# Optimization experiments

Hardware: AMD Instinct MI355X
Metric: run time of the kernel (lower is better)

Reference implementation:

```python
import jax, jax.numpy as jnp
import numpy as np

DIM = 1024
HEADS = 16
SCALE = DIM ** -0.5  # note: source scales by full dim, not head dim


def setup_inputs() -> dict:
    key = jax.random.key(0)
    k1, k2, k3 = jax.random.split(key, 3)
    b, n = 2, 2048
    x = jax.random.normal(k1, (b, n, DIM), dtype=jnp.float32)
    w_qkv = jax.random.normal(k2, (3 * DIM, DIM), dtype=jnp.float32) * (DIM ** -0.5)
    w_out = jax.random.normal(k3, (DIM, DIM), dtype=jnp.float32) * (DIM ** -0.5)
    b_out = jnp.zeros((DIM,), dtype=jnp.float32)
    return {"x": x, "w_qkv": w_qkv, "w_out": w_out, "b_out": b_out}


def reference(x, w_qkv, w_out, b_out):
    b, n, d = x.shape
    h = HEADS
    hd = d // h
    # torch Linear: y = x @ W.T
    qkv = x @ w_qkv.T  # [b, n, 3d]
    q, k, v = jnp.split(qkv, 3, axis=-1)
    # reshape to [b, h, n, hd]
    def to_heads(t):
        return t.reshape(b, n, h, hd).transpose(0, 2, 1, 3)
    q, k, v = to_heads(q), to_heads(k), to_heads(v)
    dots = jnp.einsum('bhqd,bhkd->bhqk', q, k) * SCALE
    attn = jax.nn.softmax(dots, axis=-1)
    out = jnp.einsum('bhqk,bhkd->bhqd', attn, v)
    out = out.transpose(0, 2, 1, 3).reshape(b, n, d)
    return out @ w_out.T + b_out
```

## Files before the change

### kernel.cpp

```cpp
#include <hip/hip_runtime.h>

typedef __attribute__((ext_vector_type(8))) _Float16 half8;
typedef __attribute__((ext_vector_type(4))) _Float16 half4;
typedef __attribute__((ext_vector_type(2))) __fp16 fp16x2;
typedef __attribute__((ext_vector_type(4))) float f32x4;
typedef __attribute__((ext_vector_type(4))) unsigned int u32x4;
typedef __attribute__((ext_vector_type(2))) unsigned int u32x2;

#define NSEQ 2048
#define DIMM 1024
#define NH   16
#define HD   64

typedef const void __attribute__((address_space(1))) gvoid_t;
typedef void __attribute__((address_space(3))) svoid_t;

__device__ __forceinline__ void gload_lds16(const void* g, void* l) {
  __builtin_amdgcn_global_load_lds((gvoid_t*)g, (svoid_t*)l, 16, 0, 0);
}

union H2U { fp16x2 h; unsigned int u; };

__global__ __launch_bounds__(256) void cvt_all(const float* __restrict__ x,
                                               const float* __restrict__ wqkv,
                                               const float* __restrict__ wout,
                                               _Float16* __restrict__ xh,
                                               _Float16* __restrict__ wqkvh,
                                               _Float16* __restrict__ wouth) {
  int i = blockIdx.x * 256 + threadIdx.x;
  const float* src;
  _Float16* dst;
  int off;
  if (i < 524288) { src = x; dst = xh; off = i; }
  else if (i < 917504) { src = wqkv; dst = wqkvh; off = i - 524288; }
  else { src = wout; dst = wouth; off = i - 917504; }
  const float4* p = (const float4*)src + (size_t)off * 2;
  float4 v0 = p[0], v1 = p[1];
  half8 h;
  h[0] = (_Float16)v0.x; h[1] = (_Float16)v0.y; h[2] = (_Float16)v0.z; h[3] = (_Float16)v0.w;
  h[4] = (_Float16)v1.x; h[5] = (_Float16)v1.y; h[6] = (_Float16)v1.z; h[7] = (_Float16)v1.w;
  *((half8*)dst + off) = h;
}

__device__ __forceinline__ void gemm_mainloop_q(const _Float16* __restrict__ A,
                                                const _Float16* __restrict__ B,
                                                int am0, int bn0,
                                                _Float16* As, _Float16* Bs,
                                                f32x4 acc[4][4]) {
  const int tid = threadIdx.x;
  const int w = tid >> 6, lane = tid & 63;
  const int lr = lane >> 2;
  const int lc = (lane & 3) * 8;
  const int wm = (w >> 1) * 64, wn = (w & 1) * 64;
  const int g = lane >> 4, ln = lane & 15;

#define GSTAGE_Q(buf, kk)                                                           \
  {                                                                                 \
    _Pragma("unroll")                                                               \
    for (int i = 0; i < 4; ++i) {                                                   \
      int c = w * 4 + i;                                                            \
      if (c < 8) {                                                                  \
        gload_lds16(A + (size_t)(am0 + c * 16 + lr) * 1024 + (kk) + lc,             \
                    As + (buf) * 4096 + c * 512);                                   \
      } else {                                                                      \
        int cb = c - 8;                                                             \
        gload_lds16(B + (size_t)(bn0 + cb * 16 + lr) * 1024 + (kk) + lc,            \
                    Bs + (buf) * 4096 + cb * 512);                                  \
      }                                                                             \
    }                                                                               \
  }

  GSTAGE_Q(0, 0)
  GSTAGE_Q(1, 32)
  for (int t = 0; t < 32; ++t) {
    if (t < 31) {
      asm volatile("s_waitcnt vmcnt(4)" ::: "memory");
    } else {
      asm volatile("s_waitcnt vmcnt(0)" ::: "memory");
    }
    __builtin_amdgcn_s_barrier();
    if (t < 30) GSTAGE_Q((t + 2) % 3, (t + 2) * 32);
    const _Float16* as_ = As + (t % 3) * 4096;
    const _Float16* bs_ = Bs + (t % 3) * 4096;
    half8 af[4], bf[4];
#pragma unroll
    for (int mi = 0; mi < 4; ++mi)
      af[mi] = *(const half8*)(as_ + (wm + mi * 16 + ln) * 32 + g * 8);
#pragma unroll
    for (int ni = 0; ni < 4; ++ni)
      bf[ni] = *(const half8*)(bs_ + (wn + ni * 16 + ln) * 32 + g * 8);
#pragma unroll
    for (int mi = 0; mi < 4; ++mi)
#pragma unroll
      for (int ni = 0; ni < 4; ++ni)
        acc[mi][ni] = __builtin_amdgcn_mfma_f32_16x16x32_f16(af[mi], bf[ni], acc[mi][ni], 0, 0, 0);
  }
}

union SmemQKV {
  struct { _Float16 a[3 * 128 * 32]; _Float16 b[3 * 128 * 32]; } ab;
  _Float16 t[128 * 136];
};

#define QSCALE 0.0450843450f

__global__ __launch_bounds__(256) void gemm_qkv(const _Float16* __restrict__ x,
                                                const _Float16* __restrict__ wqkv,
                                                _Float16* __restrict__ qh,
                                                _Float16* __restrict__ kh,
                                                _Float16* __restrict__ vt) {
  __shared__ SmemQKV sh;
  f32x4 acc[4][4];
#pragma unroll
  for (int i = 0; i < 4; ++i)
#pragma unroll
    for (int j = 0; j < 4; ++j) acc[i][j] = (f32x4){0.f, 0.f, 0.f, 0.f};
  const int bm = blockIdx.x, bn = blockIdx.y;
  gemm_mainloop_q(x, wqkv, bm * 128, bn * 128, sh.ab.a, sh.ab.b, acc);

  const int tid = threadIdx.x;
  const int w = tid >> 6, lane = tid & 63;
  const int g = lane >> 4, ln = lane & 15;
  const int wm = (w >> 1) * 64, wn = (w & 1) * 64;
  const int sec = bn >> 3;
  const int cbase = (bn & 7) * 128;

  if (sec < 2) {
    _Float16* dst = (sec == 0) ? qh : kh;
    const float scale = (sec == 0) ? QSCALE : 1.0f;
#pragma unroll
    for (int mi = 0; mi < 4; ++mi) {
      int row = bm * 128 + wm + mi * 16 + g * 4;
      int bidx = row >> 11, nidx = row & 2047;
#pragma unroll
      for (int ni = 0; ni < 4; ++ni) {
        int col = cbase + wn + ni * 16 + ln;
        int h = col >> 6, d = col & 63;
        _Float16* p = dst + ((size_t)(bidx * NH + h) * NSEQ + nidx) * HD + d;
#pragma unroll
        for (int r = 0; r < 4; ++r) p[r * HD] = (_Float16)(acc[mi][ni][r] * scale);
      }
    }
  } else {
    __syncthreads();
#pragma unroll
    for (int mi = 0; mi < 4; ++mi)
#pragma unroll
      for (int ni = 0; ni < 4; ++ni)
#pragma unroll
        for (int r = 0; r < 4; ++r)
          sh.t[(wn + ni * 16 + ln) * 136 + wm + mi * 16 + g * 4 + r] = (_Float16)acc[mi][ni][r];
    __syncthreads();
    const int row0 = bm * 128;
    const int bidx = row0 >> 11, n0 = row0 & 2047;
#pragma unroll
    for (int i = 0; i < 8; ++i) {
      int ci = i * 256 + tid;
      int drow = ci >> 4, nofs = (ci & 15) * 8;
      int col = cbase + drow;
      int h = col >> 6, d = col & 63;
      u32x4 val = *(const u32x4*)(sh.t + drow * 136 + nofs);
      *(u32x4*)(vt + ((size_t)(bidx * NH + h) * HD + d) * NSEQ + n0 + nofs) = val;
    }
  }
}

__global__ __launch_bounds__(256, 2) void attn_fwd(const _Float16* __restrict__ qg,
                                                   const _Float16* __restrict__ kg,
                                                   const _Float16* __restrict__ vg,
                                                   _Float16* __restrict__ ao) {
  __shared__ _Float16 Ks[3][64 * 64];
  __shared__ _Float16 Vs[3][64 * 64];
  __shared__ float Lred[2][128];

  const int bid = blockIdx.x;
  const int swz = (bid & 7) * 64 + (bid >> 3);
  const int bh = swz >> 4, qt = swz & 15;
  const int tid = threadIdx.x, w = tid >> 6, lane = tid & 63;
  const int g = lane >> 4, ln = lane & 15;
  const int sw8 = ln & 7;
  const int qh2 = w >> 1, kh2 = w & 1;

  const _Float16* qp = qg + (size_t)bh * NSEQ * HD;
  const _Float16* kp = kg + (size_t)bh * NSEQ * HD;
  const _Float16* vp = vg + (size_t)bh * HD * NSEQ;

  const int qr0 = qt * 128;

  half8 qf[4][2];
#pragma unroll
  for (int qb = 0; qb < 4; ++qb)
#pragma unroll
    for (int dk = 0; dk < 2; ++dk)
      qf[qb][dk] = *(const half8*)(qp + (size_t)(qr0 + qh2 * 64 + qb * 16 + ln) * HD + dk * 32 + g * 8);
  asm volatile("" ::: "memory");

  const int rsub = lane >> 3;
  const int csw = ((lane & 7) ^ rsub) << 3;
  const int c0 = 2 * w;
  const int R0 = c0 * 8 + rsub, R1 = R0 + 8;
  const int ks0 = 32 * (R0 >> 5) + 8 * ((R0 >> 2) & 3) + 4 * ((R0 >> 4) & 1) + (R0 & 3);
  const int ks1 = 32 * (R1 >> 5) + 8 * ((R1 >> 2) & 3) + 4 * ((R1 >> 4) & 1) + (R1 & 3);

#define STAGE(buf, tt)                                                              \
  {                                                                                 \
    const _Float16* kt_ = kp + (size_t)(tt) * 64 * HD;                              \
    gload_lds16(kt_ + (size_t)ks0 * HD + csw, &Ks[buf][c0 * 512]);                  \
    gload_lds16(kt_ + (size_t)ks1 * HD + csw, &Ks[buf][(c0 + 1) * 512]);            \
    gload_lds16(vp + (size_t)(c0 * 8 + rsub) * NSEQ + (tt) * 64 + csw,              \
                &Vs[buf][c0 * 512]);                                                \
    gload_lds16(vp + (size_t)((c0 + 1) * 8 + rsub) * NSEQ + (tt) * 64 + csw,        \
                &Vs[buf][(c0 + 1) * 512]);                                          \
  }

  STAGE(0, 0);
  STAGE(1, 1);

  float lsum[4] = {0.f, 0.f, 0.f, 0.f};
  f32x4 oacc[4][4];
#pragma unroll
  for (int sd = 0; sd < 4; ++sd)
#pragma unroll
    for (int qb = 0; qb < 4; ++qb) oacc[sd][qb] = (f32x4){0.f, 0.f, 0.f, 0.f};
  const f32x4 fz = (f32x4){0.f, 0.f, 0.f, 0.f};

#define TILE_BODY(kbuf, vbuf)                                                       \
  {                                                                                 \
    const _Float16* kb_ = (kbuf);                                                   \
    const _Float16* vb_ = (vbuf);                                                   \
    f32x4 sacc[2][4];                                                               \
    __builtin_amdgcn_s_setprio(1);                                                  \
    _Pragma("unroll")                                                               \
    for (int s = 0; s < 2; ++s) {                                                   \
      const _Float16* kr = kb_ + (kh2 * 32 + s * 16 + ln) * 64;                     \
      half8 kf0 = *(const half8*)(kr + ((g ^ sw8) << 3));                           \
      half8 kf1 = *(const half8*)(kr + (((4 + g) ^ sw8) << 3));                     \
      _Pragma("unroll")                                                             \
      for (int qb = 0; qb < 4; ++qb) {                                              \
        sacc[s][qb] = __builtin_amdgcn_mfma_f32_16x16x32_f16(kf0, qf[qb][0], fz, 0, 0, 0);          \
        sacc[s][qb] = __builtin_amdgcn_mfma_f32_16x16x32_f16(kf1, qf[qb][1], sacc[s][qb], 0, 0, 0); \
      }                                                                             \
    }                                                                               \
    __builtin_amdgcn_s_setprio(0);                                                  \
    half8 vf[4];                                                                    \
    _Pragma("unroll")                                                               \
    for (int sd = 0; sd < 4; ++sd)                                                  \
      vf[sd] = *(const half8*)(vb_ + (sd * 16 + ln) * 64 +                          \
                               (((kh2 * 4 + g) ^ sw8) << 3));                       \
    half8 pb[4];                                                                    \
    _Pragma("unroll")                                                               \
    for (int qb = 0; qb < 4; ++qb) {                                                \
      float e0 = __builtin_amdgcn_exp2f(sacc[0][qb][0]);                            \
      float e1 = __builtin_amdgcn_exp2f(sacc[0][qb][1]);                            \
      float e2 = __builtin_amdgcn_exp2f(sacc[0][qb][2]);                            \
      float e3 = __builtin_amdgcn_exp2f(sacc[0][qb][3]);                            \
      float e4 = __builtin_amdgcn_exp2f(sacc[1][qb][0]);                            \
      float e5 = __builtin_amdgcn_exp2f(sacc[1][qb][1]);                            \
      float e6 = __builtin_amdgcn_exp2f(sacc[1][qb][2]);                            \
      float e7 = __builtin_amdgcn_exp2f(sacc[1][qb][3]);                            \
      lsum[qb] += ((e0 + e1) + (e2 + e3)) + ((e4 + e5) + (e6 + e7));                \
      H2U c0_, c1_, c2_, c3_;                                                       \
      c0_.h = __builtin_amdgcn_cvt_pkrtz(e0, e1);                                   \
      c1_.h = __builtin_amdgcn_cvt_pkrtz(e2, e3);                                   \
      c2_.h = __builtin_amdgcn_cvt_pkrtz(e4, e5);                                   \
      c3_.h = __builtin_amdgcn_cvt_pkrtz(e6, e7);                                   \
      union { u32x4 u; half8 h; } pk;                                               \
      pk.u[0] = c0_.u; pk.u[1] = c1_.u; pk.u[2] = c2_.u; pk.u[3] = c3_.u;           \
      pb[qb] = pk.h;                                                                \
    }                                                                               \
    __builtin_amdgcn_s_setprio(1);                                                  \
    _Pragma("unroll")                                                               \
    for (int sd = 0; sd < 4; ++sd)                                                  \
      _Pragma("unroll")                                                             \
      for (int qb = 0; qb < 4; ++qb)                                                \
        oacc[sd][qb] = __builtin_amdgcn_mfma_f32_16x16x32_f16(vf[sd], pb[qb], oacc[sd][qb], 0, 0, 0); \
    __builtin_amdgcn_s_setprio(0);                                                  \
  }

  for (int t = 0; t < 30; ++t) {
    asm volatile("s_waitcnt vmcnt(4)" ::: "memory");
    __builtin_amdgcn_s_barrier();
    STAGE((t + 2) % 3, t + 2);
    TILE_BODY(&Ks[t % 3][0], &Vs[t % 3][0])
  }
  {
    asm volatile("s_waitcnt vmcnt(4)" ::: "memory");
    __builtin_amdgcn_s_barrier();
    TILE_BODY(&Ks[0][0], &Vs[0][0])
  }
  {
    asm volatile("s_waitcnt vmcnt(0)" ::: "memory");
    __builtin_amdgcn_s_barrier();
    TILE_BODY(&Ks[1][0], &Vs[1][0])
  }

#pragma unroll
  for (int qb = 0; qb < 4; ++qb) {
    lsum[qb] += __shfl_xor(lsum[qb], 16, 64);
    lsum[qb] += __shfl_xor(lsum[qb], 32, 64);
  }
  __syncthreads();
  float* Osh = (float*)&Ks[0][0];
  if (g == 0) {
#pragma unroll
    for (int qb = 0; qb < 4; ++qb)
      Lred[kh2][qh2 * 64 + qb * 16 + ln] = lsum[qb];
  }
  if (kh2) {
#pragma unroll
    for (int sd = 0; sd < 4; ++sd)
#pragma unroll
      for (int qb = 0; qb < 4; ++qb)
        *(f32x4*)&Osh[(qh2 * 64 + qb * 16 + ln) * 66 + sd * 16 + g * 4] = oacc[sd][qb];
  }
  __syncthreads();
  if (!kh2) {
    const int bidx = bh >> 4, h = bh & 15;
#pragma unroll
    for (int qb = 0; qb < 4; ++qb) {
      const int q = qh2 * 64 + qb * 16 + ln;
      const float inv = 1.f / (Lred[0][q] + Lred[1][q]);
      const int n = qr0 + q;
#pragma unroll
      for (int sd = 0; sd < 4; ++sd) {
        f32x4 part = *(const f32x4*)&Osh[q * 66 + sd * 16 + g * 4];
        half4 o4;
#pragma unroll
        for (int r = 0; r < 4; ++r) o4[r] = (_Float16)((oacc[sd][qb][r] + part[r]) * inv);
        *(half4*)(ao + (size_t)(bidx * NSEQ + n) * DIMM + h * HD + sd * 16 + g * 4) = o4;
      }
    }
  }
}

__global__ __launch_bounds__(256) void gemm_out(const _Float16* __restrict__ ao,
                                                const _Float16* __restrict__ wout,
                                                const float* __restrict__ bias,
                                                float* __restrict__ out) {
  __shared__ _Float16 As[3 * 128 * 32];
  __shared__ _Float16 Bs[3 * 64 * 32];
  f32x4 acc[4][2];
#pragma unroll
  for (int i = 0; i < 4; ++i)
#pragma unroll
    for (int j = 0; j < 2; ++j) acc[i][j] = (f32x4){0.f, 0.f, 0.f, 0.f};
  const int bm = blockIdx.x, bn = blockIdx.y;
  const int am0 = bm * 128, bn0 = bn * 64;

  const int tid = threadIdx.x;
  const int w = tid >> 6, lane = tid & 63;
  const int lr = lane >> 2;
  const int lc = (lane & 3) * 8;
  const int wm = (w >> 1) * 64, wn = (w & 1) * 32;
  const int g = lane >> 4, ln = lane & 15;

#define GSTAGE_O(buf, kk)                                                           \
  {                                                                                 \
    _Pragma("unroll")                                                               \
    for (int i = 0; i < 3; ++i) {                                                   \
      int c = w * 3 + i;                                                            \
      if (c < 8) {                                                                  \
        gload_lds16(ao + (size_t)(am0 + c * 16 + lr) * 1024 + (kk) + lc,            \
                    As + (buf) * 4096 + c * 512);                                   \
      } else {                                                                      \
        int cb = c - 8;                                                             \
        gload_lds16(wout + (size_t)(bn0 + cb * 16 + lr) * 1024 + (kk) + lc,         \
                    Bs + (buf) * 2048 + cb * 512);                                  \
      }                                                                             \
    }                                                                               \
  }

  GSTAGE_O(0, 0)
  GSTAGE_O(1, 32)
  for (int t = 0; t < 32; ++t) {
    if (t < 31) {
      asm volatile("s_waitcnt vmcnt(3)" ::: "memory");
    } else {
      asm volatile("s_waitcnt vmcnt(0)" ::: "memory");
    }
    __builtin_amdgcn_s_barrier();
    if (t < 30) GSTAGE_O((t + 2) % 3, (t + 2) * 32);
    const _Float16* as_ = As + (t % 3) * 4096;
    const _Float16* bs_ = Bs + (t % 3) * 2048;
    half8 af[4], bf[2];
#pragma unroll
    for (int mi = 0; mi < 4; ++mi)
      af[mi] = *(const half8*)(as_ + (wm + mi * 16 + ln) * 32 + g * 8);
#pragma unroll
    for (int ni = 0; ni < 2; ++ni)
      bf[ni] = *(const half8*)(bs_ + (wn + ni * 16 + ln) * 32 + g * 8);
#pragma unroll
    for (int mi = 0; mi < 4; ++mi)
#pragma unroll
      for (int ni = 0; ni < 2; ++ni)
        acc[mi][ni] = __builtin_amdgcn_mfma_f32_16x16x32_f16(af[mi], bf[ni], acc[mi][ni], 0, 0, 0);
  }

#pragma unroll
  for (int mi = 0; mi < 4; ++mi) {
    const int row = bm * 128 + wm + mi * 16 + g * 4;
#pragma unroll
    for (int ni = 0; ni < 2; ++ni) {
      const int col = bn * 64 + wn + ni * 16 + ln;
      const float b = bias[col];
#pragma unroll
      for (int r = 0; r < 4; ++r) out[(size_t)(row + r) * DIMM + col] = acc[mi][ni][r] + b;
    }
  }
}

extern "C" void kernel_launch(void* const* d_in, const int* in_sizes, int n_in,
                              void* d_out, int out_size, void* d_ws, size_t ws_size,
                              hipStream_t stream) {
  const float* x    = (const float*)d_in[0];
  const float* wqkv = (const float*)d_in[1];
  const float* wout = (const float*)d_in[2];
  const float* bout = (const float*)d_in[3];
  float* out = (float*)d_out;

  _Float16* ws = (_Float16*)d_ws;
  _Float16* x_h    = ws;
  _Float16* wqkv_h = ws + (4u << 20);
  _Float16* wout_h = ws + (7u << 20);
  _Float16* q_h    = ws + (8u << 20);
  _Float16* k_h    = ws + (12u << 20);
  _Float16* vt_h   = ws + (16u << 20);
  _Float16* ao_h   = ws + (20u << 20);

  cvt_all<<<dim3(4096), 256, 0, stream>>>(x, wqkv, wout, x_h, wqkv_h, wout_h);
  gemm_qkv<<<dim3(32, 24), 256, 0, stream>>>(x_h, wqkv_h, q_h, k_h, vt_h);
  attn_fwd<<<dim3(512), 256, 0, stream>>>(q_h, k_h, vt_h, ao_h);
  gemm_out<<<dim3(32, 16), 256, 0, stream>>>(ao_h, wout_h, bout, out);
}
```

Before: 105.7 us.

## Enlarge QKV GEMM tiles to 256x256 with 512 threads and swizzled LDS

The QKV projection GEMM moves from 128x128 tiles with 256 threads to 256x256 tiles with 512 threads and 8x4 MFMA accumulators per wave. It also XOR-swizzles the LDS layout to avoid bank conflicts, spreads the next-stage global loads between MFMA groups, and remaps block IDs so neighbouring blocks share operands in L2. The aim is more data reuse per load and fewer LDS conflicts. The cost is 192 blocks on a 256-CU part, so some CUs sit idle, plus higher register pressure at one block per CU.

After: 100.2 us, median of 2. 1.05x faster.

```diff
diff --git a/kernel.cpp b/kernel.cpp
--- a/kernel.cpp
+++ b/kernel.cpp
@@ -42,125 +42,136 @@
   *((half8*)dst + off) = h;
 }
 
-__device__ __forceinline__ void gemm_mainloop_q(const _Float16* __restrict__ A,
-                                                const _Float16* __restrict__ B,
-                                                int am0, int bn0,
-                                                _Float16* As, _Float16* Bs,
-                                                f32x4 acc[4][4]) {
-  const int tid = threadIdx.x;
-  const int w = tid >> 6, lane = tid & 63;
-  const int lr = lane >> 2;
-  const int lc = (lane & 3) * 8;
-  const int wm = (w >> 1) * 64, wn = (w & 1) * 64;
+#define QSCALE 0.0450843450f
+
+union SmemQ {
+  struct { _Float16 A[3 * 8192]; _Float16 B[3 * 8192]; } m;
+  _Float16 t[128 * 264];
+};
+
+__global__ __launch_bounds__(512, 1) void gemm_qkv(const _Float16* __restrict__ x,
+                                                   const _Float16* __restrict__ wqkv,
+                                                   _Float16* __restrict__ qh,
+                                                   _Float16* __restrict__ kh,
+                                                   _Float16* __restrict__ vt) {
+  __shared__ SmemQ sh;
+  const int bid = blockIdx.x;
+  const int swz = (bid & 7) * 24 + (bid >> 3);
+  const int bm = swz & 15, bn = swz >> 4;
+  const int am0 = bm * 256, bn0 = bn * 256;
+  const int tid = threadIdx.x, w = tid >> 6, lane = tid & 63;
   const int g = lane >> 4, ln = lane & 15;
-
-#define GSTAGE_Q(buf, kk)                                                           \
+  const int wmq = (w >> 2) * 128, wnq = (w & 3) * 64;
+
+  const int srl = tid >> 2;
+  const int ssl = (tid & 3) ^ ((srl >> 1) & 3);
+  const int dsto = tid * 8;
+
+#define QSTG(buf, kt, ht)                                                           \
   {                                                                                 \
-    _Pragma("unroll")                                                               \
-    for (int i = 0; i < 4; ++i) {                                                   \
-      int c = w * 4 + i;                                                            \
-      if (c < 8) {                                                                  \
-        gload_lds16(A + (size_t)(am0 + c * 16 + lr) * 1024 + (kk) + lc,             \
-                    As + (buf) * 4096 + c * 512);                                   \
-      } else {                                                                      \
-        int cb = c - 8;                                                             \
-        gload_lds16(B + (size_t)(bn0 + cb * 16 + lr) * 1024 + (kk) + lc,            \
-                    Bs + (buf) * 4096 + cb * 512);                                  \
-      }                                                                             \
+    if ((ht) < 2) {                                                                 \
+      gload_lds16(x + (size_t)(am0 + (ht) * 128 + srl) * 1024 + (kt) * 32 + ssl * 8,\
+                  sh.m.A + (buf) * 8192 + (ht) * 4096 + dsto);                      \
+    } else {                                                                        \
+      gload_lds16(wqkv + (size_t)(bn0 + ((ht) - 2) * 128 + srl) * 1024 +            \
+                      (kt) * 32 + ssl * 8,                                          \
+                  sh.m.B + (buf) * 8192 + ((ht) - 2) * 4096 + dsto);                \
     }                                                                               \
   }
 
-  GSTAGE_Q(0, 0)
-  GSTAGE_Q(1, 32)
+  f32x4 acc[8][4];
+#pragma unroll
+  for (int i = 0; i < 8; ++i)
+#pragma unroll
+    for (int j = 0; j < 4; ++j) acc[i][j] = (f32x4){0.f, 0.f, 0.f, 0.f};
+
+#pragma unroll
+  for (int ht = 0; ht < 4; ++ht) QSTG(0, 0, ht)
+#pragma unroll
+  for (int ht = 0; ht < 4; ++ht) QSTG(1, 1, ht)
+
   for (int t = 0; t < 32; ++t) {
+    const int buf = t % 3;
+    const int sbuf = (t + 2) % 3;
     if (t < 31) {
       asm volatile("s_waitcnt vmcnt(4)" ::: "memory");
     } else {
       asm volatile("s_waitcnt vmcnt(0)" ::: "memory");
     }
     __builtin_amdgcn_s_barrier();
-    if (t < 30) GSTAGE_Q((t + 2) % 3, (t + 2) * 32);
-    const _Float16* as_ = As + (t % 3) * 4096;
-    const _Float16* bs_ = Bs + (t % 3) * 4096;
-    half8 af[4], bf[4];
-#pragma unroll
-    for (int mi = 0; mi < 4; ++mi)
-      af[mi] = *(const half8*)(as_ + (wm + mi * 16 + ln) * 32 + g * 8);
-#pragma unroll
-    for (int ni = 0; ni < 4; ++ni)
-      bf[ni] = *(const half8*)(bs_ + (wn + ni * 16 + ln) * 32 + g * 8);
-#pragma unroll
-    for (int mi = 0; mi < 4; ++mi)
-#pragma unroll
-      for (int ni = 0; ni < 4; ++ni)
-        acc[mi][ni] = __builtin_amdgcn_mfma_f32_16x16x32_f16(af[mi], bf[ni], acc[mi][ni], 0, 0, 0);
-  }
-}
-
-union SmemQKV {
-  struct { _Float16 a[3 * 128 * 32]; _Float16 b[3 * 128 * 32]; } ab;
-  _Float16 t[128 * 136];
-};
-
-#define QSCALE 0.0450843450f
-
-__global__ __launch_bounds__(256) void gemm_qkv(const _Float16* __restrict__ x,
-                                                const _Float16* __restrict__ wqkv,
-                                                _Float16* __restrict__ qh,
-                                                _Float16* __restrict__ kh,
-                                                _Float16* __restrict__ vt) {
-  __shared__ SmemQKV sh;
-  f32x4 acc[4][4];
-#pragma unroll
-  for (int i = 0; i < 4; ++i)
-#pragma unroll
-    for (int j = 0; j < 4; ++j) acc[i][j] = (f32x4){0.f, 0.f, 0.f, 0.f};
-  const int bm = blockIdx.x, bn = blockIdx.y;
-  gemm_mainloop_q(x, wqkv, bm * 128, bn * 128, sh.ab.a, sh.ab.b, acc);
-
-  const int tid = threadIdx.x;
-  const int w = tid >> 6, lane = tid & 63;
-  const int g = lane >> 4, ln = lane & 15;
-  const int wm = (w >> 1) * 64, wn = (w & 1) * 64;
-  const int sec = bn >> 3;
-  const int cbase = (bn & 7) * 128;
+    const _Float16* Ab = sh.m.A + buf * 8192;
+    const _Float16* Bb = sh.m.B + buf * 8192;
+    half8 bf[4];
+#pragma unroll
+    for (int ni = 0; ni < 4; ++ni) {
+      const int r = wnq + ni * 16 + ln;
+      bf[ni] = *(const half8*)(Bb + r * 32 + ((g ^ ((r >> 1) & 3)) << 3));
+    }
+#pragma unroll
+    for (int p = 0; p < 4; ++p) {
+      const int r0 = wmq + (2 * p) * 16 + ln;
+      const int r1 = wmq + (2 * p + 1) * 16 + ln;
+      half8 af0 = *(const half8*)(Ab + r0 * 32 + ((g ^ ((r0 >> 1) & 3)) << 3));
+      half8 af1 = *(const half8*)(Ab + r1 * 32 + ((g ^ ((r1 >> 1) & 3)) << 3));
+      __builtin_amdgcn_s_setprio(1);
+#pragma unroll
+      for (int ni = 0; ni < 4; ++ni) {
+        acc[2 * p][ni]     = __builtin_amdgcn_mfma_f32_16x16x32_f16(af0, bf[ni], acc[2 * p][ni], 0, 0, 0);
+        acc[2 * p + 1][ni] = __builtin_amdgcn_mfma_f32_16x16x32_f16(af1, bf[ni], acc[2 * p + 1][ni], 0, 0, 0);
+      }
+      __builtin_amdgcn_s_setprio(0);
+      if (t < 30) QSTG(sbuf, t + 2, p)
+      if (p < 3) __builtin_amdgcn_s_barrier();
+    }
+  }
+
+  const int sec = bn >> 2;
+  const int cbase = (bn & 3) * 256;
 
   if (sec < 2) {
     _Float16* dst = (sec == 0) ? qh : kh;
     const float scale = (sec == 0) ? QSCALE : 1.0f;
 #pragma unroll
-    for (int mi = 0; mi < 4; ++mi) {
-      int row = bm * 128 + wm + mi * 16 + g * 4;
-      int bidx = row >> 11, nidx = row & 2047;
+    for (int mi = 0; mi < 8; ++mi) {
+      const int row = am0 + wmq + mi * 16 + g * 4;
+      const int bidx = row >> 11, nidx = row & 2047;
 #pragma unroll
       for (int ni = 0; ni < 4; ++ni) {
-        int col = cbase + wn + ni * 16 + ln;
-        int h = col >> 6, d = col & 63;
+        const int col = cbase + wnq + ni * 16 + ln;
+        const int h = col >> 6, d = col & 63;
         _Float16* p = dst + ((size_t)(bidx * NH + h) * NSEQ + nidx) * HD + d;
 #pragma unroll
         for (int r = 0; r < 4; ++r) p[r * HD] = (_Float16)(acc[mi][ni][r] * scale);
       }
     }
   } else {
-    __syncthreads();
-#pragma unroll
-    for (int mi = 0; mi < 4; ++mi)
-#pragma unroll
-      for (int ni = 0; ni < 4; ++ni)
-#pragma unroll
-        for (int r = 0; r < 4; ++r)
-          sh.t[(wn + ni * 16 + ln) * 136 + wm + mi * 16 + g * 4 + r] = (_Float16)acc[mi][ni][r];
-    __syncthreads();
-    const int row0 = bm * 128;
-    const int bidx = row0 >> 11, n0 = row0 & 2047;
-#pragma unroll
-    for (int i = 0; i < 8; ++i) {
-      int ci = i * 256 + tid;
-      int drow = ci >> 4, nofs = (ci & 15) * 8;
-      int col = cbase + drow;
-      int h = col >> 6, d = col & 63;
-      u32x4 val = *(const u32x4*)(sh.t + drow * 136 + nofs);
-      *(u32x4*)(vt + ((size_t)(bidx * NH + h) * HD + d) * NSEQ + n0 + nofs) = val;
+    const int bidx = bm >> 3;
+    const int n0 = (bm * 256) & 2047;
+#pragma unroll
+    for (int hc = 0; hc < 2; ++hc) {
+      __syncthreads();
+      if (((w & 3) >> 1) == hc) {
+#pragma unroll
+        for (int mi = 0; mi < 8; ++mi)
+#pragma unroll
+          for (int ni = 0; ni < 4; ++ni) {
+            const int cl = wnq + ni * 16 + ln - hc * 128;
+            const int rowl = wmq + mi * 16 + g * 4;
+#pragma unroll
+            for (int r = 0; r < 4; ++r)
+              sh.t[cl * 264 + rowl + r] = (_Float16)acc[mi][ni][r];
+          }
+      }
+      __syncthreads();
+#pragma unroll
+      for (int i = 0; i < 8; ++i) {
+        const int ci = i * 512 + tid;
+        const int cl = ci >> 5, npos = (ci & 31) * 8;
+        const int col = cbase + hc * 128 + cl;
+        const int h = col >> 6, d = col & 63;
+        u32x4 v = *(const u32x4*)(sh.t + cl * 264 + npos);
+        *(u32x4*)(vt + ((size_t)(bidx * NH + h) * HD + d) * NSEQ + n0 + npos) = v;
+      }
     }
   }
 }
@@ -202,7 +213,7 @@
   const int ks0 = 32 * (R0 >> 5) + 8 * ((R0 >> 2) & 3) + 4 * ((R0 >> 4) & 1) + (R0 & 3);
   const int ks1 = 32 * (R1 >> 5) + 8 * ((R1 >> 2) & 3) + 4 * ((R1 >> 4) & 1) + (R1 & 3);
 
-#define STAGE(buf, tt)                                                              \
+#define ASTAGE(buf, tt)                                                             \
   {                                                                                 \
     const _Float16* kt_ = kp + (size_t)(tt) * 64 * HD;                              \
     gload_lds16(kt_ + (size_t)ks0 * HD + csw, &Ks[buf][c0 * 512]);                  \
@@ -213,8 +224,8 @@
                 &Vs[buf][(c0 + 1) * 512]);                                          \
   }
 
-  STAGE(0, 0);
-  STAGE(1, 1);
+  ASTAGE(0, 0);
+  ASTAGE(1, 1);
 
   float lsum[4] = {0.f, 0.f, 0.f, 0.f};
   f32x4 oacc[4][4];
@@ -280,7 +291,7 @@
   for (int t = 0; t < 30; ++t) {
     asm volatile("s_waitcnt vmcnt(4)" ::: "memory");
     __builtin_amdgcn_s_barrier();
-    STAGE((t + 2) % 3, t + 2);
+    ASTAGE((t + 2) % 3, t + 2);
     TILE_BODY(&Ks[t % 3][0], &Vs[t % 3][0])
   }
   {
@@ -428,7 +439,7 @@
   _Float16* ao_h   = ws + (20u << 20);
 
   cvt_all<<<dim3(4096), 256, 0, stream>>>(x, wqkv, wout, x_h, wqkv_h, wout_h);
-  gemm_qkv<<<dim3(32, 24), 256, 0, stream>>>(x_h, wqkv_h, q_h, k_h, vt_h);
+  gemm_qkv<<<dim3(192), 512, 0, stream>>>(x_h, wqkv_h, q_h, k_h, vt_h);
   attn_fwd<<<dim3(512), 256, 0, stream>>>(q_h, k_h, vt_h, ao_h);
   gemm_out<<<dim3(32, 16), 256, 0, stream>>>(ao_h, wout_h, bout, out);
 }
```
